# Optimization experiments

Measured on AMD Instinct MI355X. Metric: run time of the kernel, lower is better.

Reference implementation:

```python
import jax, jax.numpy as jnp
import numpy as np

N = 50000      # nodes
E = 800000     # edges (avg degree 16)
IN = 64        # in_channels
H = 128        # hidden_channels
OUT = 64       # out_channels
NS = 10        # n_samples
EPS = 1e-5     # BatchNorm eps


def _sage_conv(x, src, dst, Wl, bl, Wr):
    # PyG SAGEConv (mean aggr): lin_l(mean_neighbors) + lin_r(x)
    n = x.shape[0]
    deg = jax.ops.segment_sum(jnp.ones(src.shape[0], x.dtype), dst, num_segments=n)
    agg = jax.ops.segment_sum(x[src], dst, num_segments=n) / jnp.clip(deg, 1.0)[:, None]
    return agg @ Wl + bl + x @ Wr


def _batchnorm(x, gamma, beta):
    # training-mode BN forward (batch statistics), deterministic
    m = x.mean(axis=0)
    v = x.var(axis=0)
    return (x - m) * jax.lax.rsqrt(v + EPS) * gamma + beta


def setup_inputs() -> dict:
    key = jax.random.key(0)
    ks = jax.random.split(key, 40)
    w = lambda k, shape: (jax.random.normal(k, shape, jnp.float32) * 0.05)
    inp = {
        "x": jax.random.normal(ks[0], (N, IN), jnp.float32),
        "edge_index": jax.random.randint(ks[1], (2, E), 0, N, dtype=jnp.int32),
        "batch": jnp.zeros((N,), jnp.int32),
        "noise": jax.random.normal(ks[2], (NS, N, OUT), jnp.float32),
        # encoder1: SAGEConv(IN,H) + BN(H)
        "We1l": w(ks[3], (IN, H)), "be1": jnp.zeros((H,), jnp.float32), "We1r": w(ks[4], (IN, H)),
        "g1": jnp.ones((H,), jnp.float32), "b1": jnp.zeros((H,), jnp.float32),
        # encoder2: SAGEConv(H,2H) + BN(2H) + SAGEConv(2H,2*OUT)
        "We2l": w(ks[5], (H, 2 * H)), "be2": jnp.zeros((2 * H,), jnp.float32), "We2r": w(ks[6], (H, 2 * H)),
        "g2": jnp.ones((2 * H,), jnp.float32), "b2": jnp.zeros((2 * H,), jnp.float32),
        "We3l": w(ks[7], (2 * H, 2 * OUT)), "be3": jnp.zeros((2 * OUT,), jnp.float32), "We3r": w(ks[8], (2 * H, 2 * OUT)),
        # x1_transform: Linear(H, IN)
        "Wt": w(ks[9], (H, IN)), "bt": jnp.zeros((IN,), jnp.float32),
        # decoder1: Linear(OUT+IN, H) + BN(H); decoder2: Linear(H, IN)
        "Wd1": w(ks[10], (OUT + IN, H)), "bd1": jnp.zeros((H,), jnp.float32),
        "gd": jnp.ones((H,), jnp.float32), "bd": jnp.zeros((H,), jnp.float32),
        "Wd2": w(ks[11], (H, IN)), "bd2": jnp.zeros((IN,), jnp.float32),
        # SAGPooling score GNN = GraphConv(H, 1): lin_rel (bias) + lin_root (no bias)
        "Wp_rel": w(ks[12], (H, 1)), "bp": jnp.zeros((1,), jnp.float32), "Wp_root": w(ks[13], (H, 1)),
    }
    return inp


def reference(x, edge_index, batch, noise,
              We1l, be1, We1r, g1, b1,
              We2l, be2, We2r, g2, b2,
              We3l, be3, We3r,
              Wt, bt, Wd1, bd1, gd, bd, Wd2, bd2,
              Wp_rel, bp, Wp_root):
    src, dst = edge_index[0], edge_index[1]

    # ---- encode ----
    x1 = _batchnorm(jax.nn.relu(_sage_conv(x, src, dst, We1l, be1, We1r)), g1, b1)
    x2 = _batchnorm(jax.nn.relu(_sage_conv(x1, src, dst, We2l, be2, We2r)), g2, b2)
    ms = _sage_conv(x2, src, dst, We3l, be3, We3r)        # [N, 2*OUT]
    mean, log_std = ms[:, :OUT], ms[:, OUT:]

    # ---- reparameterize: avg of n_samples draws == mean + std * mean(eps) ----
    z = mean + jnp.exp(log_std) * noise.mean(axis=0)

    # ---- decode ----
    x1t = x1 @ Wt + bt                                    # [N, IN]
    h = jax.nn.relu(jnp.concatenate([z, x1t], axis=-1) @ Wd1 + bd1)
    h = _batchnorm(h, gd, bd)
    reconstruction = h @ Wd2 + bd2                        # [N, IN]

    # ---- SAGPooling (ratio=0.5) on x1 ----
    agg = jax.ops.segment_sum(x1[src], dst, num_segments=N)   # GraphConv add-aggr
    score = jnp.tanh((agg @ Wp_rel + bp + x1 @ Wp_root)[:, 0])  # [N]
    k = N // 2
    _, perm = jax.lax.top_k(score, k)                     # kept node indices (desc score)

    keep = jnp.zeros((N,), bool).at[perm].set(True)
    newidx = jnp.zeros((N,), jnp.int32).at[perm].set(jnp.arange(k, dtype=jnp.int32))
    edge_mask = keep[src] & keep[dst]                     # edges surviving the pooling
    ei_cg = newidx[edge_index]                            # [2, E], valid where edge_mask
    # unpool: map coarse indices back to original node ids; -1 marks dropped edges
    edge_index_unpooled = jnp.where(edge_mask[None, :], perm[ei_cg].astype(jnp.int32), -1)
    x_unpooled = x1[perm]                                 # [k, H]

    return (reconstruction, x_unpooled, edge_index_unpooled, edge_mask, mean, log_std, x1)
```

## Files before the change

### kernel.cpp

```cpp
#include <hip/hip_runtime.h>
#include <hip/hip_bf16.h>
#include <math.h>

#define NN 50000
#define EE 800000
#define KHALF 25000
#define NSAMP 1024
#define NBK (NSAMP+1)

typedef short bf16x8 __attribute__((ext_vector_type(8)));
typedef short sh4 __attribute__((ext_vector_type(4)));
typedef float f32x4 __attribute__((ext_vector_type(4)));

static __device__ inline unsigned short f2bf(float f){
  __hip_bfloat16 h = __float2bfloat16(f);
  return __builtin_bit_cast(unsigned short, h);
}
static __device__ inline float bf2f(unsigned short u){
  unsigned int x = ((unsigned int)u)<<16;
  return __builtin_bit_cast(float, x);
}

__global__ void k_hist(const int* __restrict__ dst, int* __restrict__ cnt, int E){
  int i = blockIdx.x*blockDim.x + threadIdx.x;
  if(i<E) atomicAdd(&cnt[dst[i]], 1);
}

__global__ void k_scan(const int* __restrict__ deg, int* __restrict__ rowptr, int n){
  __shared__ int sm[1024];
  int t = threadIdx.x;
  int chunk = (n + 1023) >> 10;
  int b = t*chunk; int e = b+chunk; if(b>n) b=n; if(e>n) e=n;
  int s=0;
  for(int i=b;i<e;i++) s += deg[i];
  sm[t]=s; __syncthreads();
  for(int off=1; off<1024; off<<=1){
    int add = (t>=off)? sm[t-off] : 0;
    __syncthreads();
    sm[t] += add;
    __syncthreads();
  }
  int run = sm[t]-s;
  for(int i=b;i<e;i++){ rowptr[i]=run; run += deg[i]; }
  if(t==1023) rowptr[n]=sm[1023];
}

__global__ void k_fill(const int* __restrict__ src, const int* __restrict__ dst,
                       const int* __restrict__ rowptr, int* __restrict__ cnt,
                       int* __restrict__ csr, int E){
  int i = blockIdx.x*blockDim.x + threadIdx.x;
  if(i<E){
    int d = dst[i];
    int p = rowptr[d] + atomicAdd(&cnt[d],1);
    csr[p] = src[i];
  }
}

template<typename AccT, typename OT, int F, int VW>
__global__ void k_segmean(const float* __restrict__ x, const int* __restrict__ csr,
                          const int* __restrict__ rowptr, OT* __restrict__ out, int n){
  int gid = blockIdx.x*blockDim.x + threadIdx.x;
  int node = gid >> 6; int lane = gid & 63;
  if(node>=n) return;
  int b = rowptr[node], e = rowptr[node+1];
  AccT acc[VW];
  #pragma unroll
  for(int k=0;k<VW;k++) acc[k]=(AccT)0;
  const float* xp = x + lane*VW;
  for(int j=b;j<e;j++){
    const float* row = xp + (long)csr[j]*F;
    if(VW==1){
      acc[0] += (AccT)row[0];
    } else if(VW==2){
      float2 v = *(const float2*)row;
      acc[0]+=(AccT)v.x; acc[1]+=(AccT)v.y;
    } else {
      float4 v = *(const float4*)row;
      acc[0]+=(AccT)v.x; acc[1]+=(AccT)v.y; acc[2]+=(AccT)v.z; acc[3]+=(AccT)v.w;
    }
  }
  int d = e-b; if(d<1) d=1;
  AccT inv = (AccT)1 / (AccT)d;
  #pragma unroll
  for(int k=0;k<VW;k++) out[(long)node*F + lane*VW + k] = (OT)(acc[k]*inv);
}

__global__ void k_segmean_bf(const unsigned short* __restrict__ xb,
                             const int* __restrict__ csr, const int* __restrict__ rowptr,
                             float* __restrict__ out, int n){
  int gid = blockIdx.x*blockDim.x + threadIdx.x;
  int node = gid >> 6; int lane = gid & 63;
  if(node>=n) return;
  int b = rowptr[node], e = rowptr[node+1];
  float a0=0.f, a1=0.f;
  const unsigned short* xp = xb + lane*2;
  for(int j=b;j<e;j++){
    unsigned int u = *(const unsigned int*)(xp + (long)csr[j]*128);
    a0 += bf2f((unsigned short)(u & 0xffff));
    a1 += bf2f((unsigned short)(u >> 16));
  }
  int d=e-b; if(d<1)d=1;
  float inv = 1.f/(float)d;
  float2 r; r.x=a0*inv; r.y=a1*inv;
  *(float2*)(out + (long)node*128 + lane*2) = r;
}

__global__ void k_segmean_ms(const unsigned short* __restrict__ T3,
                             const float* __restrict__ msr,
                             const int* __restrict__ csr, const int* __restrict__ rowptr,
                             float* __restrict__ omean, float* __restrict__ olstd, int n){
  int gid = blockIdx.x*blockDim.x + threadIdx.x;
  int node = gid >> 6; int lane = gid & 63;
  if(node>=n) return;
  int b = rowptr[node], e = rowptr[node+1];
  float a0=0.f, a1=0.f;
  const unsigned short* xp = T3 + lane*2;
  for(int j=b;j<e;j++){
    unsigned int u = *(const unsigned int*)(xp + (long)csr[j]*128);
    a0 += bf2f((unsigned short)(u & 0xffff));
    a1 += bf2f((unsigned short)(u >> 16));
  }
  int d=e-b; if(d<1)d=1;
  float inv = 1.f/(float)d;
  float2 mv = *(const float2*)(msr + (long)node*128 + lane*2);
  float2 r; r.x = a0*inv + mv.x; r.y = a1*inv + mv.y;
  int c0 = lane*2;
  if(c0 < 64) *(float2*)(omean + (long)node*64 + c0)      = r;
  else        *(float2*)(olstd + (long)node*64 + (c0-64)) = r;
}

static __device__ inline void stage_A_bf16(const float* __restrict__ P, int K, int k0,
                                           int m0, int M, int t,
                                           const float* __restrict__ bnsc,
                                           const float* __restrict__ bnsh,
                                           short* Ah, short* Al, bool bn){
  #pragma unroll
  for(int i=0;i<8;i++){
    int f4  = t + i*256;
    int row = f4 >> 4, c4 = f4 & 15;
    int gr  = m0 + row;
    float4 v = make_float4(0.f,0.f,0.f,0.f);
    if(gr < M) v = *(const float4*)(P + (long)gr*K + k0 + c4*4);
    if(bn){
      int kc = k0 + c4*4;
      v.x = v.x*bnsc[kc]   + bnsh[kc];
      v.y = v.y*bnsc[kc+1] + bnsh[kc+1];
      v.z = v.z*bnsc[kc+2] + bnsh[kc+2];
      v.w = v.w*bnsc[kc+3] + bnsh[kc+3];
    }
    unsigned short h0=f2bf(v.x), h1=f2bf(v.y), h2=f2bf(v.z), h3=f2bf(v.w);
    sh4 hi = (sh4){(short)h0,(short)h1,(short)h2,(short)h3};
    sh4 lo = (sh4){(short)f2bf(v.x-bf2f(h0)), (short)f2bf(v.y-bf2f(h1)),
                   (short)f2bf(v.z-bf2f(h2)), (short)f2bf(v.w-bf2f(h3))};
    int byte = (row*128 + c4*8) ^ ((row&7)<<4);
    *(sh4*)((char*)Ah + byte) = hi;
    *(sh4*)((char*)Al + byte) = lo;
  }
}

static __device__ inline void stage_B_bf16(const float* __restrict__ W, int J, int k0,
                                           int n0, int t, short* Bh, short* Bl){
  int n = t & 63, k4 = (t>>6)<<2;
  #pragma unroll
  for(int i=0;i<4;i++){
    int kb = i*16 + k4;
    const float* wp = W + (long)(k0+kb)*J + n0 + n;
    float w0 = wp[0], w1 = wp[J], w2 = wp[2*J], w3 = wp[3*J];
    unsigned short h0=f2bf(w0), h1=f2bf(w1), h2=f2bf(w2), h3=f2bf(w3);
    sh4 hi = (sh4){(short)h0,(short)h1,(short)h2,(short)h3};
    sh4 lo = (sh4){(short)f2bf(w0-bf2f(h0)), (short)f2bf(w1-bf2f(h1)),
                   (short)f2bf(w2-bf2f(h2)), (short)f2bf(w3-bf2f(h3))};
    int byte = (n*128 + kb*2) ^ ((n&7)<<4);
    *(sh4*)((char*)Bh + byte) = hi;
    *(sh4*)((char*)Bl + byte) = lo;
  }
}

__global__ __launch_bounds__(256) void k_gemm_bf16s(
    const float* __restrict__ A, const float* __restrict__ W1, int K1,
    const float* __restrict__ X, const float* __restrict__ W2, int K2,
    const float* __restrict__ bias, float* __restrict__ out,
    int M, int J, int relu,
    const float* __restrict__ bnsc, const float* __restrict__ bnsh)
{
  __shared__ __align__(16) short Ah[128*64];
  __shared__ __align__(16) short Al[128*64];
  __shared__ __align__(16) short Bh[64*64];
  __shared__ __align__(16) short Bl[64*64];
  const int m0 = blockIdx.x*128, n0 = blockIdx.y*64;
  const int t = threadIdx.x;
  const int lane = t & 63, wid = t >> 6;
  const int wm = wid >> 1, wn = wid & 1;

  f32x4 acc[4][2];
  #pragma unroll
  for(int i=0;i<4;i++)
    #pragma unroll
    for(int j=0;j<2;j++) acc[i][j] = (f32x4){0.f,0.f,0.f,0.f};

  const int ns1 = K1 >> 6;
  const int ns2 = X ? (K2 >> 6) : 0;
  for(int s=0; s<ns1+ns2; ++s){
    const float* P; const float* W; int K, k0;
    if(s < ns1){ P = A; W = W1; K = K1; k0 = s*64; }
    else       { P = X; W = W2; K = K2; k0 = (s-ns1)*64; }
    const bool bn = (bnsc != nullptr) && (s < ns1);

    stage_A_bf16(P, K, k0, m0, M, t, bnsc, bnsh, Ah, Al, bn);
    stage_B_bf16(W, J, k0, n0, t, Bh, Bl);
    __syncthreads();

    #pragma unroll
    for(int kk=0;kk<2;kk++){
      int kb = kk*32 + (lane>>4)*8;
      bf16x8 ahf[4], alf[4], bhf[2], blf[2];
      #pragma unroll
      for(int mf=0; mf<4; mf++){
        int r = wm*64 + mf*16 + (lane&15);
        int byte = (r*128 + kb*2) ^ ((r&7)<<4);
        ahf[mf] = *(const bf16x8*)((const char*)Ah + byte);
        alf[mf] = *(const bf16x8*)((const char*)Al + byte);
      }
      #pragma unroll
      for(int nf=0; nf<2; nf++){
        int n = wn*32 + nf*16 + (lane&15);
        int byte = (n*128 + kb*2) ^ ((n&7)<<4);
        bhf[nf] = *(const bf16x8*)((const char*)Bh + byte);
        blf[nf] = *(const bf16x8*)((const char*)Bl + byte);
      }
      #pragma unroll
      for(int mf=0; mf<4; mf++)
        #pragma unroll
        for(int nf=0; nf<2; nf++){
          acc[mf][nf] = __builtin_amdgcn_mfma_f32_16x16x32_bf16(ahf[mf], bhf[nf], acc[mf][nf], 0,0,0);
          acc[mf][nf] = __builtin_amdgcn_mfma_f32_16x16x32_bf16(ahf[mf], blf[nf], acc[mf][nf], 0,0,0);
          acc[mf][nf] = __builtin_amdgcn_mfma_f32_16x16x32_bf16(alf[mf], bhf[nf], acc[mf][nf], 0,0,0);
        }
    }
    __syncthreads();
  }

  #pragma unroll
  for(int mf=0; mf<4; mf++){
    #pragma unroll
    for(int nf=0; nf<2; nf++){
      int col = n0 + wn*32 + nf*16 + (lane&15);
      #pragma unroll
      for(int q=0;q<4;q++){
        int row = m0 + wm*64 + mf*16 + (lane>>4)*4 + q;
        if(row >= M) continue;
        float v = acc[mf][nf][q] + (bias ? bias[col] : 0.f);
        if(relu) v = fmaxf(v, 0.f);
        out[(long)row*J + col] = v;
      }
    }
  }
}

__global__ __launch_bounds__(256) void k_gemm_bf16s_2w(
    const float* __restrict__ A,
    const float* __restrict__ Wa, const float* __restrict__ Wb,
    const float* __restrict__ biasb,
    unsigned short* __restrict__ outa, float* __restrict__ outb,
    int M, int K,
    const float* __restrict__ bnsc, const float* __restrict__ bnsh)
{
  __shared__ __align__(16) short Ah[128*64];
  __shared__ __align__(16) short Al[128*64];
  __shared__ __align__(16) short Bh[64*64];
  __shared__ __align__(16) short Bl[64*64];
  const bool sel = blockIdx.y >= 2;
  const float* W = sel ? Wb : Wa;
  const int m0 = blockIdx.x*128, n0 = (blockIdx.y & 1)*64;
  const int t = threadIdx.x;
  const int lane = t & 63, wid = t >> 6;
  const int wm = wid >> 1, wn = wid & 1;

  f32x4 acc[4][2];
  #pragma unroll
  for(int i=0;i<4;i++)
    #pragma unroll
    for(int j=0;j<2;j++) acc[i][j] = (f32x4){0.f,0.f,0.f,0.f};

  const int ns1 = K >> 6;
  for(int s=0; s<ns1; ++s){
    int k0 = s*64;
    stage_A_bf16(A, K, k0, m0, M, t, bnsc, bnsh, Ah, Al, bnsc!=nullptr);
    stage_B_bf16(W, 128, k0, n0, t, Bh, Bl);
    __syncthreads();

    #pragma unroll
    for(int kk=0;kk<2;kk++){
      int kb = kk*32 + (lane>>4)*8;
      bf16x8 ahf[4], alf[4], bhf[2], blf[2];
      #pragma unroll
      for(int mf=0; mf<4; mf++){
        int r = wm*64 + mf*16 + (lane&15);
        int byte = (r*128 + kb*2) ^ ((r&7)<<4);
        ahf[mf] = *(const bf16x8*)((const char*)Ah + byte);
        alf[mf] = *(const bf16x8*)((const char*)Al + byte);
      }
      #pragma unroll
      for(int nf=0; nf<2; nf++){
        int n = wn*32 + nf*16 + (lane&15);
        int byte = (n*128 + kb*2) ^ ((n&7)<<4);
        bhf[nf] = *(const bf16x8*)((const char*)Bh + byte);
        blf[nf] = *(const bf16x8*)((const char*)Bl + byte);
      }
      #pragma unroll
      for(int mf=0; mf<4; mf++)
        #pragma unroll
        for(int nf=0; nf<2; nf++){
          acc[mf][nf] = __builtin_amdgcn_mfma_f32_16x16x32_bf16(ahf[mf], bhf[nf], acc[mf][nf], 0,0,0);
          acc[mf][nf] = __builtin_amdgcn_mfma_f32_16x16x32_bf16(ahf[mf], blf[nf], acc[mf][nf], 0,0,0);
          acc[mf][nf] = __builtin_amdgcn_mfma_f32_16x16x32_bf16(alf[mf], bhf[nf], acc[mf][nf], 0,0,0);
        }
    }
    __syncthreads();
  }

  #pragma unroll
  for(int mf=0; mf<4; mf++){
    #pragma unroll
    for(int nf=0; nf<2; nf++){
      int col = n0 + wn*32 + nf*16 + (lane&15);
      #pragma unroll
      for(int q=0;q<4;q++){
        int row = m0 + wm*64 + mf*16 + (lane>>4)*4 + q;
        if(row >= M) continue;
        if(sel){
          outb[(long)row*128 + col] = acc[mf][nf][q] + biasb[col];
        } else {
          outa[(long)row*128 + col] = f2bf(acc[mf][nf][q]);
        }
      }
    }
  }
}

__global__ __launch_bounds__(256) void k_gemm_c1(
    const double* __restrict__ A1, const float* __restrict__ X,
    const float* __restrict__ W1, const float* __restrict__ W2,
    const float* __restrict__ bias, double* __restrict__ out, int M)
{
  __shared__ double Asd[32*67];
  __shared__ float  Wsf[32*66];
  const int m0 = blockIdx.x*64, n0 = blockIdx.y*64;
  const int t = threadIdx.x;
  const int tm = t & 15, tn = t >> 4;
  double acc[4][4];
  #pragma unroll
  for(int i=0;i<4;i++)
    #pragma unroll
    for(int j=0;j<4;j++) acc[i][j]=0.0;

  for(int pair=0; pair<2; pair++){
    const float* Wp = pair ? W2 : W1;
    for(int k0=0; k0<64; k0+=32){
      #pragma unroll
      for(int i=0;i<8;i++){
        int idx = t + i*256;
        int r = idx >> 5, c = idx & 31;
        int gr = m0 + r;
        double v = 0.0;
        if(gr<M) v = pair ? (double)X[(long)gr*64 + k0 + c] : A1[(long)gr*64 + k0 + c];
        Asd[c*67 + r] = v;
      }
      #pragma unroll
      for(int i=0;i<8;i++){
        int idx = t + i*256;
        int kk = idx >> 6, n = idx & 63;
        Wsf[kk*66 + n] = Wp[(k0+kk)*128 + n0 + n];
      }
      __syncthreads();
      #pragma unroll
      for(int kk=0;kk<32;kk++){
        double a0=Asd[kk*67 + tm],    a1=Asd[kk*67 + tm+16];
        double a2=Asd[kk*67 + tm+32], a3=Asd[kk*67 + tm+48];
        double w0=(double)Wsf[kk*66 + tn*4+0], w1=(double)Wsf[kk*66 + tn*4+1];
        double w2=(double)Wsf[kk*66 + tn*4+2], w3=(double)Wsf[kk*66 + tn*4+3];
        acc[0][0] += a0*w0; acc[0][1] += a0*w1; acc[0][2] += a0*w2; acc[0][3] += a0*w3;
        acc[1][0] += a1*w0; acc[1][1] += a1*w1; acc[1][2] += a1*w2; acc[1][3] += a1*w3;
        acc[2][0] += a2*w0; acc[2][1] += a2*w1; acc[2][2] += a2*w2; acc[2][3] += a2*w3;
        acc[3][0] += a3*w0; acc[3][1] += a3*w1; acc[3][2] += a3*w2; acc[3][3] += a3*w3;
      }
      __syncthreads();
    }
  }
  #pragma unroll
  for(int i=0;i<4;i++){
    int gr = m0 + tm + 16*i;
    if(gr>=M) continue;
    #pragma unroll
    for(int j=0;j<4;j++){
      int gc = n0 + tn*4 + j;
      double v = acc[i][j] + (double)bias[gc];
      if(v<0.0) v=0.0;
      out[(long)gr*128 + gc] = v;
    }
  }
}

__global__ void k_wfold(const float* __restrict__ Wt, const float* __restrict__ bt,
                        const float* __restrict__ Wd1, const float* __restrict__ bd1,
                        float* __restrict__ Wc, float* __restrict__ bc){
  int j = threadIdx.x;
  int i = blockIdx.x;
  float s;
  if(i < 128){
    s = 0.f;
    for(int k=0;k<64;k++) s += Wt[i*64+k] * Wd1[(64+k)*128 + j];
    Wc[i*128+j] = s;
  } else {
    s = bd1[j];
    for(int k=0;k<64;k++) s += bt[k] * Wd1[(64+k)*128 + j];
    bc[j] = s;
  }
}

template<typename T>
__global__ void k_colstats(const T* __restrict__ x, int M, int J,
                           double* __restrict__ ps, double* __restrict__ pq){
  int c = threadIdx.x; int b = blockIdx.x, B = gridDim.x;
  int rows = (M + B - 1)/B;
  int r0 = b*rows, r1 = r0+rows; if(r1>M) r1=M;
  double s=0.0,q=0.0;
  for(int r=r0;r<r1;r++){ double v = (double)x[(long)r*J + c]; s+=v; q+=v*v; }
  ps[(long)b*J+c]=s; pq[(long)b*J+c]=q;
}

__global__ void k_bnfinal(const double* __restrict__ ps, const double* __restrict__ pq,
                          int B, int J, int M, const float* __restrict__ g,
                          const float* __restrict__ bta,
                          double* __restrict__ sc, double* __restrict__ sh,
                          float* __restrict__ sc32, float* __restrict__ sh32){
  int c = threadIdx.x; if(c>=J) return;
  double s=0.0,q=0.0;
  for(int b=0;b<B;b++){ s+=ps[(long)b*J+c]; q+=pq[(long)b*J+c]; }
  double m = s/M; double v = q/M - m*m;
  double inv = 1.0/sqrt(v + 1e-5);
  double a = (double)g[c]*inv;
  sc[c]=a; sh[c]=(double)bta[c] - m*a;
  sc32[c]=(float)a; sh32[c]=(float)((double)bta[c] - m*a);
}

__global__ void k_bntr(const double* __restrict__ xp,
                       const double* __restrict__ sc, const double* __restrict__ sh,
                       const float* __restrict__ wrel, const float* __restrict__ wroot,
                       float* __restrict__ o32, unsigned short* __restrict__ obf,
                       double* __restrict__ t, double* __restrict__ r, int n){
  int gid = blockIdx.x*blockDim.x + threadIdx.x;
  int node = gid>>6, lane = gid&63;
  if(node>=n) return;
  long base = (long)node*128;
  double v0 = xp[base+lane]   *sc[lane]    + sh[lane];
  double v1 = xp[base+lane+64]*sc[lane+64] + sh[lane+64];
  float f0 = (float)v0, f1 = (float)v1;
  o32[base+lane]    = f0;
  o32[base+lane+64] = f1;
  obf[base+lane]    = f2bf(f0);
  obf[base+lane+64] = f2bf(f1);
  double tv = v0*(double)wrel[lane]  + v1*(double)wrel[lane+64];
  double rv = v0*(double)wroot[lane] + v1*(double)wroot[lane+64];
  for(int off=32; off>0; off>>=1){
    tv += __shfl_xor(tv, off);
    rv += __shfl_xor(rv, off);
  }
  if(lane==0){ t[node]=tv; r[node]=rv; }
}

__global__ void k_z(const float* __restrict__ mean, const float* __restrict__ lstd,
                    const float* __restrict__ noise, float* __restrict__ z, int total4){
  int i = blockIdx.x*blockDim.x + threadIdx.x;
  if(i>=total4) return;
  const float4* m4 = (const float4*)mean;
  const float4* l4 = (const float4*)lstd;
  const float4* n4 = (const float4*)noise;
  float4 m = m4[i], l = l4[i];
  float nx=0.f, ny=0.f, nz=0.f, nw=0.f;
  #pragma unroll
  for(int s=0;s<10;s++){
    float4 v = n4[(long)s*total4 + i];
    nx+=v.x; ny+=v.y; nz+=v.z; nw+=v.w;
  }
  float4 o;
  o.x = (float)((double)m.x + exp((double)l.x)*((double)nx*0.1));
  o.y = (float)((double)m.y + exp((double)l.y)*((double)ny*0.1));
  o.z = (float)((double)m.z + exp((double)l.z)*((double)nz*0.1));
  o.w = (float)((double)m.w + exp((double)l.w)*((double)nw*0.1));
  ((float4*)z)[i] = o;
}

__global__ void k_score(const double* __restrict__ t, const double* __restrict__ r,
                        const int* __restrict__ csr, const int* __restrict__ rowptr,
                        const float* __restrict__ bp,
                        unsigned long long* __restrict__ key, int n){
  int i = blockIdx.x*blockDim.x + threadIdx.x;
  if(i>=n) return;
  double s = (double)bp[0] + r[i];
  int b=rowptr[i], e=rowptr[i+1];
  for(int j=b;j<e;j++) s += t[csr[j]];
  double sc = tanh(s) + 0.0;
  long long u = __double_as_longlong(sc);
  unsigned long long uu = (unsigned long long)u;
  key[i] = (u < 0) ? ~uu : (uu ^ 0x8000000000000000ULL);
}

__global__ void k_sample_sort(const unsigned long long* __restrict__ key,
                              unsigned long long* __restrict__ samp){
  __shared__ unsigned long long sm[NSAMP];
  int t = threadIdx.x;
  sm[t] = key[t*48];
  __syncthreads();
  for(int k=2; k<=NSAMP; k<<=1){
    for(int j=k>>1; j>0; j>>=1){
      int l = t ^ j;
      if(l > t){
        unsigned long long a = sm[t], b = sm[l];
        bool up = ((t & k) == 0);
        if(up ? (a > b) : (a < b)){ sm[t]=b; sm[l]=a; }
      }
      __syncthreads();
    }
  }
  samp[t] = sm[t];
}

__global__ __launch_bounds__(256) void k_bucket_assign(
    const unsigned long long* __restrict__ key,
    const unsigned long long* __restrict__ samp,
    int* __restrict__ bucket, int* __restrict__ bcnt, int n){
  __shared__ unsigned long long sm[NSAMP];
  for(int u=threadIdx.x; u<NSAMP; u+=256) sm[u] = samp[u];
  __syncthreads();
  int i = blockIdx.x*256 + threadIdx.x;
  if(i>=n) return;
  unsigned long long ki = key[i];
  int lo=0, hi=NSAMP;
  while(lo<hi){ int mid=(lo+hi)>>1; if(sm[mid] < ki) lo=mid+1; else hi=mid; }
  bucket[i]=lo;
  atomicAdd(&bcnt[lo],1);
}

__global__ void k_bucket_fill(const int* __restrict__ bucket,
                              const int* __restrict__ bstart, int* __restrict__ bfill,
                              int* __restrict__ blist, int n){
  int i = blockIdx.x*blockDim.x + threadIdx.x;
  if(i>=n) return;
  int b = bucket[i];
  int p = bstart[b] + atomicAdd(&bfill[b],1);
  blist[p] = i;
}

__global__ __launch_bounds__(256) void k_bucket_rank(
    const unsigned long long* __restrict__ key,
    const int* __restrict__ blist, const int* __restrict__ bstart,
    int n, int k, int* __restrict__ keep, int* __restrict__ perm){
  __shared__ unsigned long long skey[2048];
  __shared__ int sidx[2048];
  int b = blockIdx.x;
  int s0 = bstart[b], s1 = bstart[b+1];
  int m = s1 - s0;
  if(m<=0) return;
  int above = n - s1;
  if(m <= 2048){
    for(int u=threadIdx.x; u<m; u+=256){ int ii=blist[s0+u]; sidx[u]=ii; skey[u]=key[ii]; }
    __syncthreads();
    for(int u=threadIdx.x; u<m; u+=256){
      unsigned long long ki = skey[u]; int ii = sidx[u];
      int c = 0;
      for(int v=0; v<m; v++){
        unsigned long long kv = skey[v];
        c += ((kv > ki) || (kv == ki && sidx[v] < ii)) ? 1 : 0;
      }
      int rank = above + c;
      int kp = (rank < k) ? 1 : 0;
      keep[ii] = kp;
      if(kp) perm[rank] = ii;
    }
  } else {
    for(int u=threadIdx.x; u<m; u+=256){
      int ii = blist[s0+u];
      unsigned long long ki = key[ii];
      int c=0;
      for(int v=0; v<m; v++){
        int jj = blist[s0+v];
        unsigned long long kv = key[jj];
        c += ((kv > ki) || (kv == ki && jj < ii)) ? 1 : 0;
      }
      int rank = above + c;
      int kp = (rank < k) ? 1 : 0;
      keep[ii] = kp;
      if(kp) perm[rank] = ii;
    }
  }
}

__global__ void k_unpool(const float* __restrict__ x1, const int* __restrict__ perm,
                         float* __restrict__ out, int k){
  int i = blockIdx.x*blockDim.x + threadIdx.x;
  if(i >= k*128) return;
  int r = i>>7, c = i&127;
  out[i] = x1[(long)perm[r]*128 + c];
}

__global__ void k_edgeout(const int* __restrict__ src, const int* __restrict__ dst,
                          const int* __restrict__ keep, float* __restrict__ o2,
                          float* __restrict__ o3, int E){
  int e = blockIdx.x*blockDim.x + threadIdx.x;
  if(e>=E) return;
  int s=src[e], d=dst[e];
  bool m = keep[s] && keep[d];
  o2[e]   = m ? (float)s : -1.f;
  o2[E+e] = m ? (float)d : -1.f;
  o3[e]   = m ? 1.f : 0.f;
}

extern "C" void kernel_launch(void* const* d_in, const int* in_sizes, int n_in,
                              void* d_out, int out_size, void* d_ws, size_t ws_size,
                              hipStream_t stream){
  const float* x     = (const float*)d_in[0];
  const int*   ei    = (const int*)d_in[1];
  const float* noise = (const float*)d_in[3];
  const float* We1l  = (const float*)d_in[4];
  const float* be1   = (const float*)d_in[5];
  const float* We1r  = (const float*)d_in[6];
  const float* g1    = (const float*)d_in[7];
  const float* b1    = (const float*)d_in[8];
  const float* We2l  = (const float*)d_in[9];
  const float* be2   = (const float*)d_in[10];
  const float* We2r  = (const float*)d_in[11];
  const float* g2    = (const float*)d_in[12];
  const float* b2    = (const float*)d_in[13];
  const float* We3l  = (const float*)d_in[14];
  const float* be3   = (const float*)d_in[15];
  const float* We3r  = (const float*)d_in[16];
  const float* Wt    = (const float*)d_in[17];
  const float* bt    = (const float*)d_in[18];
  const float* Wd1   = (const float*)d_in[19];
  const float* bd1   = (const float*)d_in[20];
  const float* gd    = (const float*)d_in[21];
  const float* bd    = (const float*)d_in[22];
  const float* Wd2   = (const float*)d_in[23];
  const float* bd2   = (const float*)d_in[24];
  const float* Wprel = (const float*)d_in[25];
  const float* bp    = (const float*)d_in[26];
  const float* Wproot= (const float*)d_in[27];

  const int* src = ei;
  const int* dst = ei + EE;

  float* out   = (float*)d_out;
  float* o_rec  = out;
  float* o_xun  = out + 3200000;
  float* o_eiu  = out + 6400000;
  float* o_mask = out + 8000000;
  float* o_mean = out + 8800000;
  float* o_lstd = out + 12000000;
  float* o_x1   = out + 15200000;

  char* w = (char*)d_ws;
  size_t off = 0;
  auto alloc = [&](size_t bytes)->char*{
    char* p = w + off; off += (bytes + 255) & ~(size_t)255; return p;
  };
  int*    csr  = (int*)   alloc((size_t)EE*4);
  int*    rowp = (int*)   alloc((size_t)(NN+1)*4);
  int*    cnt  = (int*)   alloc((size_t)NN*4);
  char*   B3   =          alloc((size_t)NN*128*8);
  char*   B4   =          alloc((size_t)NN*64*8);
  char*   B5   =          alloc((size_t)NN*256*4);
  double* t_   = (double*)alloc((size_t)NN*8);
  double* r_   = (double*)alloc((size_t)NN*8);
  unsigned long long* key_ = (unsigned long long*)alloc((size_t)NN*8);
  int*    keep = (int*)   alloc((size_t)NN*4);
  int*    perm = (int*)   alloc((size_t)KHALF*4);
  double* ps   = (double*)alloc((size_t)240*256*8);
  double* pq   = (double*)alloc((size_t)240*256*8);
  double* bnsc = (double*)alloc(256*8);
  double* bnsh = (double*)alloc(256*8);
  float*  sc1f = (float*) alloc(256*4);
  float*  sh1f = (float*) alloc(256*4);
  float*  sc2f = (float*) alloc(256*4);
  float*  sh2f = (float*) alloc(256*4);
  float*  scdf = (float*) alloc(256*4);
  float*  shdf = (float*) alloc(256*4);
  float*  Wc   = (float*) alloc((size_t)128*128*4);
  float*  bc   = (float*) alloc(128*4);
  unsigned long long* samp = (unsigned long long*)alloc((size_t)NSAMP*8);
  int*    bucket = (int*) alloc((size_t)NN*4);
  int*    bcnt   = (int*) alloc((size_t)NBK*4);
  int*    bstart = (int*) alloc((size_t)(NBK+1)*4);
  int*    bfill  = (int*) alloc((size_t)NBK*4);
  int*    blist  = (int*) alloc((size_t)NN*4);
  (void)in_sizes; (void)n_in; (void)out_size; (void)ws_size;

  double* A1  = (double*)B4;
  double* x1p = (double*)B3;
  float*  A2  = (float*)B4;
  float*  x2  = (float*)B3;
  unsigned short* x1bf = (unsigned short*)B5;
  unsigned short* T3   = (unsigned short*)B5;
  float*  msr = (float*)(B5 + (size_t)NN*128*4);
  float*  zb  = (float*)B5;
  float*  h   = (float*)B4;

  const int GX = (NN+127)/128;

  hipMemsetAsync(cnt, 0, (size_t)NN*4, stream);
  k_hist<<<(EE+255)/256,256,0,stream>>>(dst, cnt, EE);
  k_wfold<<<129,128,0,stream>>>(Wt, bt, Wd1, bd1, Wc, bc);
  k_scan<<<1,1024,0,stream>>>(cnt, rowp, NN);
  hipMemsetAsync(cnt, 0, (size_t)NN*4, stream);
  k_fill<<<(EE+255)/256,256,0,stream>>>(src, dst, rowp, cnt, csr, EE);

  k_segmean<double,double,64,1><<<(NN+3)/4,256,0,stream>>>(x, csr, rowp, A1, NN);
  { dim3 g((NN+63)/64, 2);
    k_gemm_c1<<<g,256,0,stream>>>(A1, x, We1l, We1r, be1, x1p, NN); }
  k_colstats<double><<<240,128,0,stream>>>(x1p, NN, 128, ps, pq);
  k_bnfinal<<<1,128,0,stream>>>(ps,pq,240,128,NN,g1,b1,bnsc,bnsh,sc1f,sh1f);
  k_bntr<<<(NN+3)/4,256,0,stream>>>(x1p, bnsc, bnsh, Wprel, Wproot, o_x1, x1bf, t_, r_, NN);

  k_segmean_bf<<<(NN+3)/4,256,0,stream>>>(x1bf, csr, rowp, A2, NN);
  { dim3 g(GX, 4);
    k_gemm_bf16s<<<g,256,0,stream>>>(A2, We2l, 128, o_x1, We2r, 128, be2, x2, NN, 256, 1, nullptr, nullptr); }
  k_colstats<float><<<240,256,0,stream>>>(x2, NN, 256, ps, pq);
  k_bnfinal<<<1,256,0,stream>>>(ps,pq,240,256,NN,g2,b2,bnsc,bnsh,sc2f,sh2f);

  { dim3 g(GX, 4);
    k_gemm_bf16s_2w<<<g,256,0,stream>>>(x2, We3l, We3r, be3, T3, msr, NN, 256, sc2f, sh2f); }
  k_segmean_ms<<<(NN+3)/4,256,0,stream>>>(T3, msr, csr, rowp, o_mean, o_lstd, NN);

  k_z<<<(800000+255)/256,256,0,stream>>>(o_mean, o_lstd, noise, zb, 800000);
  { dim3 g(GX, 2);
    k_gemm_bf16s<<<g,256,0,stream>>>(zb, Wd1, 64, o_x1, Wc, 128, bc, h, NN, 128, 1, nullptr, nullptr); }
  k_colstats<float><<<240,128,0,stream>>>(h, NN, 128, ps, pq);
  k_bnfinal<<<1,128,0,stream>>>(ps,pq,240,128,NN,gd,bd,bnsc,bnsh,scdf,shdf);
  { dim3 g(GX, 1);
    k_gemm_bf16s<<<g,256,0,stream>>>(h, Wd2, 128, nullptr, nullptr, 0, bd2, o_rec, NN, 64, 0, scdf, shdf); }

  k_score<<<(NN+255)/256,256,0,stream>>>(t_, r_, csr, rowp, bp, key_, NN);
  k_sample_sort<<<1,1024,0,stream>>>(key_, samp);
  hipMemsetAsync(bcnt, 0, (size_t)NBK*4, stream);
  k_bucket_assign<<<(NN+255)/256,256,0,stream>>>(key_, samp, bucket, bcnt, NN);
  k_scan<<<1,1024,0,stream>>>(bcnt, bstart, NBK);
  hipMemsetAsync(bfill, 0, (size_t)NBK*4, stream);
  k_bucket_fill<<<(NN+255)/256,256,0,stream>>>(bucket, bstart, bfill, blist, NN);
  k_bucket_rank<<<NBK,256,0,stream>>>(key_, blist, bstart, NN, KHALF, keep, perm);
  k_unpool<<<(KHALF*128+255)/256,256,0,stream>>>(o_x1, perm, o_xun, KHALF);
  k_edgeout<<<(EE+255)/256,256,0,stream>>>(src, dst, keep, o_eiu, o_mask, EE);
}
```

Measured before the change: 1.220 ms.

## Pre-split activations and weights into bf16 hi/lo planes before GEMMs

```diff
diff --git a/kernel.cpp b/kernel.cpp
--- a/kernel.cpp
+++ b/kernel.cpp
@@ -9,7 +9,8 @@
 #define NBK (NSAMP+1)
 
 typedef short bf16x8 __attribute__((ext_vector_type(8)));
-typedef short sh4 __attribute__((ext_vector_type(4)));
+typedef unsigned short us8 __attribute__((ext_vector_type(8)));
+typedef unsigned short us4 __attribute__((ext_vector_type(4)));
 typedef float f32x4 __attribute__((ext_vector_type(4)));
 
 static __device__ inline unsigned short f2bf(float f){
@@ -69,25 +70,17 @@
   const float* xp = x + lane*VW;
   for(int j=b;j<e;j++){
     const float* row = xp + (long)csr[j]*F;
-    if(VW==1){
-      acc[0] += (AccT)row[0];
-    } else if(VW==2){
-      float2 v = *(const float2*)row;
-      acc[0]+=(AccT)v.x; acc[1]+=(AccT)v.y;
-    } else {
-      float4 v = *(const float4*)row;
-      acc[0]+=(AccT)v.x; acc[1]+=(AccT)v.y; acc[2]+=(AccT)v.z; acc[3]+=(AccT)v.w;
-    }
+    acc[0] += (AccT)row[0];
   }
   int d = e-b; if(d<1) d=1;
   AccT inv = (AccT)1 / (AccT)d;
-  #pragma unroll
-  for(int k=0;k<VW;k++) out[(long)node*F + lane*VW + k] = (OT)(acc[k]*inv);
-}
-
-__global__ void k_segmean_bf(const unsigned short* __restrict__ xb,
-                             const int* __restrict__ csr, const int* __restrict__ rowptr,
-                             float* __restrict__ out, int n){
+  out[(long)node*F + lane] = (OT)(acc[0]*inv);
+}
+
+__global__ void k_segmean_bfp(const unsigned short* __restrict__ xb,
+                              const int* __restrict__ csr, const int* __restrict__ rowptr,
+                              unsigned short* __restrict__ a2h, unsigned short* __restrict__ a2l,
+                              int n){
   int gid = blockIdx.x*blockDim.x + threadIdx.x;
   int node = gid >> 6; int lane = gid & 63;
   if(node>=n) return;
@@ -101,8 +94,12 @@
   }
   int d=e-b; if(d<1)d=1;
   float inv = 1.f/(float)d;
-  float2 r; r.x=a0*inv; r.y=a1*inv;
-  *(float2*)(out + (long)node*128 + lane*2) = r;
+  float rx = a0*inv, ry = a1*inv;
+  unsigned short hx=f2bf(rx), hy=f2bf(ry);
+  unsigned short lx=f2bf(rx-bf2f(hx)), ly=f2bf(ry-bf2f(hy));
+  long o = (long)node*128 + lane*2;
+  *(unsigned int*)(a2h + o) = (unsigned int)hx | ((unsigned int)hy<<16);
+  *(unsigned int*)(a2l + o) = (unsigned int)lx | ((unsigned int)ly<<16);
 }
 
 __global__ void k_segmean_ms(const unsigned short* __restrict__ T3,
@@ -129,59 +126,52 @@
   else        *(float2*)(olstd + (long)node*64 + (c0-64)) = r;
 }
 
-static __device__ inline void stage_A_bf16(const float* __restrict__ P, int K, int k0,
-                                           int m0, int M, int t,
-                                           const float* __restrict__ bnsc,
-                                           const float* __restrict__ bnsh,
-                                           short* Ah, short* Al, bool bn){
-  #pragma unroll
-  for(int i=0;i<8;i++){
-    int f4  = t + i*256;
-    int row = f4 >> 4, c4 = f4 & 15;
+static __device__ inline void stage_A_ps(const unsigned short* __restrict__ AH,
+                                         const unsigned short* __restrict__ AL,
+                                         int K, int k0, int m0, int M, int t,
+                                         short* Ah, short* Al){
+  #pragma unroll
+  for(int i=0;i<4;i++){
+    int f8 = t + i*256;
+    int row = f8 >> 3, c8 = f8 & 7;
     int gr  = m0 + row;
-    float4 v = make_float4(0.f,0.f,0.f,0.f);
-    if(gr < M) v = *(const float4*)(P + (long)gr*K + k0 + c4*4);
-    if(bn){
-      int kc = k0 + c4*4;
-      v.x = v.x*bnsc[kc]   + bnsh[kc];
-      v.y = v.y*bnsc[kc+1] + bnsh[kc+1];
-      v.z = v.z*bnsc[kc+2] + bnsh[kc+2];
-      v.w = v.w*bnsc[kc+3] + bnsh[kc+3];
-    }
-    unsigned short h0=f2bf(v.x), h1=f2bf(v.y), h2=f2bf(v.z), h3=f2bf(v.w);
-    sh4 hi = (sh4){(short)h0,(short)h1,(short)h2,(short)h3};
-    sh4 lo = (sh4){(short)f2bf(v.x-bf2f(h0)), (short)f2bf(v.y-bf2f(h1)),
-                   (short)f2bf(v.z-bf2f(h2)), (short)f2bf(v.w-bf2f(h3))};
-    int byte = (row*128 + c4*8) ^ ((row&7)<<4);
-    *(sh4*)((char*)Ah + byte) = hi;
-    *(sh4*)((char*)Al + byte) = lo;
-  }
-}
-
-static __device__ inline void stage_B_bf16(const float* __restrict__ W, int J, int k0,
-                                           int n0, int t, short* Bh, short* Bl){
-  int n = t & 63, k4 = (t>>6)<<2;
-  #pragma unroll
-  for(int i=0;i<4;i++){
-    int kb = i*16 + k4;
-    const float* wp = W + (long)(k0+kb)*J + n0 + n;
-    float w0 = wp[0], w1 = wp[J], w2 = wp[2*J], w3 = wp[3*J];
-    unsigned short h0=f2bf(w0), h1=f2bf(w1), h2=f2bf(w2), h3=f2bf(w3);
-    sh4 hi = (sh4){(short)h0,(short)h1,(short)h2,(short)h3};
-    sh4 lo = (sh4){(short)f2bf(w0-bf2f(h0)), (short)f2bf(w1-bf2f(h1)),
-                   (short)f2bf(w2-bf2f(h2)), (short)f2bf(w3-bf2f(h3))};
+    us8 vh = (us8){0,0,0,0,0,0,0,0};
+    us8 vl = (us8){0,0,0,0,0,0,0,0};
+    if(gr < M){
+      long base = (long)gr*K + k0 + c8*8;
+      vh = *(const us8*)(AH + base);
+      vl = *(const us8*)(AL + base);
+    }
+    int byte = (row*128 + c8*16) ^ ((row&7)<<4);
+    *(us8*)((char*)Ah + byte) = vh;
+    *(us8*)((char*)Al + byte) = vl;
+  }
+}
+
+static __device__ inline void stage_B_ps(const unsigned short* __restrict__ WH,
+                                         const unsigned short* __restrict__ WL,
+                                         int K, int k0, int n0, int t,
+                                         short* Bh, short* Bl){
+  int n = t & 63, k8 = (t>>6)<<3;
+  #pragma unroll
+  for(int i=0;i<2;i++){
+    int kb = i*32 + k8;
+    long base = (long)(n0+n)*K + k0 + kb;
+    us8 vh = *(const us8*)(WH + base);
+    us8 vl = *(const us8*)(WL + base);
     int byte = (n*128 + kb*2) ^ ((n&7)<<4);
-    *(sh4*)((char*)Bh + byte) = hi;
-    *(sh4*)((char*)Bl + byte) = lo;
-  }
-}
-
-__global__ __launch_bounds__(256) void k_gemm_bf16s(
-    const float* __restrict__ A, const float* __restrict__ W1, int K1,
-    const float* __restrict__ X, const float* __restrict__ W2, int K2,
+    *(us8*)((char*)Bh + byte) = vh;
+    *(us8*)((char*)Bl + byte) = vl;
+  }
+}
+
+__global__ __launch_bounds__(256) void k_gemm_ps(
+    const unsigned short* __restrict__ AH, const unsigned short* __restrict__ AL, int K1,
+    const unsigned short* __restrict__ XH, const unsigned short* __restrict__ XL, int K2,
+    const unsigned short* __restrict__ W1H, const unsigned short* __restrict__ W1L,
+    const unsigned short* __restrict__ W2H, const unsigned short* __restrict__ W2L,
     const float* __restrict__ bias, float* __restrict__ out,
-    int M, int J, int relu,
-    const float* __restrict__ bnsc, const float* __restrict__ bnsh)
+    int M, int J, int relu)
 {
   __shared__ __align__(16) short Ah[128*64];
   __shared__ __align__(16) short Al[128*64];
@@ -199,15 +189,14 @@
     for(int j=0;j<2;j++) acc[i][j] = (f32x4){0.f,0.f,0.f,0.f};
 
   const int ns1 = K1 >> 6;
-  const int ns2 = X ? (K2 >> 6) : 0;
+  const int ns2 = XH ? (K2 >> 6) : 0;
   for(int s=0; s<ns1+ns2; ++s){
-    const float* P; const float* W; int K, k0;
-    if(s < ns1){ P = A; W = W1; K = K1; k0 = s*64; }
-    else       { P = X; W = W2; K = K2; k0 = (s-ns1)*64; }
-    const bool bn = (bnsc != nullptr) && (s < ns1);
-
-    stage_A_bf16(P, K, k0, m0, M, t, bnsc, bnsh, Ah, Al, bn);
-    stage_B_bf16(W, J, k0, n0, t, Bh, Bl);
+    const unsigned short *PH, *PL, *WH, *WL; int K, k0;
+    if(s < ns1){ PH=AH; PL=AL; K=K1; k0=s*64; WH=W1H; WL=W1L; }
+    else       { PH=XH; PL=XL; K=K2; k0=(s-ns1)*64; WH=W2H; WL=W2L; }
+
+    stage_A_ps(PH, PL, K, k0, m0, M, t, Ah, Al);
+    stage_B_ps(WH, WL, K, k0, n0, t, Bh, Bl);
     __syncthreads();
 
     #pragma unroll
@@ -257,20 +246,20 @@
   }
 }
 
-__global__ __launch_bounds__(256) void k_gemm_bf16s_2w(
-    const float* __restrict__ A,
-    const float* __restrict__ Wa, const float* __restrict__ Wb,
+__global__ __launch_bounds__(256) void k_gemm_ps2w(
+    const unsigned short* __restrict__ AH, const unsigned short* __restrict__ AL, int K,
+    const unsigned short* __restrict__ WaH, const unsigned short* __restrict__ WaL,
+    const unsigned short* __restrict__ WbH, const unsigned short* __restrict__ WbL,
     const float* __restrict__ biasb,
-    unsigned short* __restrict__ outa, float* __restrict__ outb,
-    int M, int K,
-    const float* __restrict__ bnsc, const float* __restrict__ bnsh)
+    unsigned short* __restrict__ outa, float* __restrict__ outb, int M)
 {
   __shared__ __align__(16) short Ah[128*64];
   __shared__ __align__(16) short Al[128*64];
   __shared__ __align__(16) short Bh[64*64];
   __shared__ __align__(16) short Bl[64*64];
   const bool sel = blockIdx.y >= 2;
-  const float* W = sel ? Wb : Wa;
+  const unsigned short* WH = sel ? WbH : WaH;
+  const unsigned short* WL = sel ? WbL : WaL;
   const int m0 = blockIdx.x*128, n0 = (blockIdx.y & 1)*64;
   const int t = threadIdx.x;
   const int lane = t & 63, wid = t >> 6;
@@ -282,11 +271,11 @@
     #pragma unroll
     for(int j=0;j<2;j++) acc[i][j] = (f32x4){0.f,0.f,0.f,0.f};
 
-  const int ns1 = K >> 6;
-  for(int s=0; s<ns1; ++s){
+  const int ns = K >> 6;
+  for(int s=0; s<ns; ++s){
     int k0 = s*64;
-    stage_A_bf16(A, K, k0, m0, M, t, bnsc, bnsh, Ah, Al, bnsc!=nullptr);
-    stage_B_bf16(W, 128, k0, n0, t, Bh, Bl);
+    stage_A_ps(AH, AL, K, k0, m0, M, t, Ah, Al);
+    stage_B_ps(WH, WL, K, k0, n0, t, Bh, Bl);
     __syncthreads();
 
     #pragma unroll
@@ -328,17 +317,14 @@
       for(int q=0;q<4;q++){
         int row = m0 + wm*64 + mf*16 + (lane>>4)*4 + q;
         if(row >= M) continue;
-        if(sel){
-          outb[(long)row*128 + col] = acc[mf][nf][q] + biasb[col];
-        } else {
-          outa[(long)row*128 + col] = f2bf(acc[mf][nf][q]);
-        }
-      }
-    }
-  }
-}
-
-__global__ __launch_bounds__(256) void k_gemm_c1(
+        if(sel) outb[(long)row*128 + col] = acc[mf][nf][q] + biasb[col];
+        else    outa[(long)row*128 + col] = f2bf(acc[mf][nf][q]);
+      }
+    }
+  }
+}
+
+__global__ __launch_bounds__(256,5) void k_gemm_c1(
     const double* __restrict__ A1, const float* __restrict__ X,
     const float* __restrict__ W1, const float* __restrict__ W2,
     const float* __restrict__ bias, double* __restrict__ out, int M)
@@ -403,18 +389,53 @@
 
 __global__ void k_wfold(const float* __restrict__ Wt, const float* __restrict__ bt,
                         const float* __restrict__ Wd1, const float* __restrict__ bd1,
-                        float* __restrict__ Wc, float* __restrict__ bc){
+                        unsigned short* __restrict__ WcTh, unsigned short* __restrict__ WcTl,
+                        float* __restrict__ bc){
   int j = threadIdx.x;
   int i = blockIdx.x;
-  float s;
   if(i < 128){
-    s = 0.f;
+    float s = 0.f;
     for(int k=0;k<64;k++) s += Wt[i*64+k] * Wd1[(64+k)*128 + j];
-    Wc[i*128+j] = s;
+    unsigned short h = f2bf(s);
+    WcTh[j*128 + i] = h;
+    WcTl[j*128 + i] = f2bf(s - bf2f(h));
   } else {
-    s = bd1[j];
+    float s = bd1[j];
     for(int k=0;k<64;k++) s += bt[k] * Wd1[(64+k)*128 + j];
     bc[j] = s;
+  }
+}
+
+static __device__ inline void wsplit1(const float* __restrict__ W, int kshift, int J,
+                                      unsigned short* __restrict__ oh,
+                                      unsigned short* __restrict__ ol, int idx){
+  int total = J << kshift;
+  if(idx >= total) return;
+  int K = 1 << kshift;
+  int n = idx >> kshift, k = idx & (K-1);
+  float v = W[k*J + n];
+  unsigned short h = f2bf(v);
+  oh[idx] = h;
+  ol[idx] = f2bf(v - bf2f(h));
+}
+
+__global__ void k_wsplit(const float* We2l, const float* We2r,
+                         const float* We3l, const float* We3r,
+                         const float* Wd1, const float* Wd2,
+                         unsigned short* e2lh, unsigned short* e2ll,
+                         unsigned short* e2rh, unsigned short* e2rl,
+                         unsigned short* e3lh, unsigned short* e3ll,
+                         unsigned short* e3rh, unsigned short* e3rl,
+                         unsigned short* d1h, unsigned short* d1l,
+                         unsigned short* d2h, unsigned short* d2l){
+  int idx = blockIdx.x*256 + threadIdx.x;
+  switch(blockIdx.y){
+    case 0: wsplit1(We2l, 7, 256, e2lh, e2ll, idx); break;
+    case 1: wsplit1(We2r, 7, 256, e2rh, e2rl, idx); break;
+    case 2: wsplit1(We3l, 8, 128, e3lh, e3ll, idx); break;
+    case 3: wsplit1(We3r, 8, 128, e3rh, e3rl, idx); break;
+    case 4: wsplit1(Wd1,  6, 128, d1h,  d1l,  idx); break;
+    case 5: wsplit1(Wd2,  7, 64,  d2h,  d2l,  idx); break;
   }
 }
 
@@ -444,10 +465,31 @@
   sc32[c]=(float)a; sh32[c]=(float)((double)bta[c] - m*a);
 }
 
+__global__ void k_bnsplit(const float* __restrict__ x, const float* __restrict__ sc,
+                          const float* __restrict__ sh,
+                          unsigned short* __restrict__ oh, unsigned short* __restrict__ ol,
+                          int total4, int Jm){
+  int i = blockIdx.x*256 + threadIdx.x;
+  if(i>=total4) return;
+  float4 v = ((const float4*)x)[i];
+  int c = (i*4) & Jm;
+  v.x = v.x*sc[c]   + sh[c];
+  v.y = v.y*sc[c+1] + sh[c+1];
+  v.z = v.z*sc[c+2] + sh[c+2];
+  v.w = v.w*sc[c+3] + sh[c+3];
+  unsigned short h0=f2bf(v.x), h1=f2bf(v.y), h2=f2bf(v.z), h3=f2bf(v.w);
+  us4 hi = (us4){h0,h1,h2,h3};
+  us4 lo = (us4){f2bf(v.x-bf2f(h0)), f2bf(v.y-bf2f(h1)),
+                 f2bf(v.z-bf2f(h2)), f2bf(v.w-bf2f(h3))};
+  ((us4*)oh)[i] = hi;
+  ((us4*)ol)[i] = lo;
+}
+
 __global__ void k_bntr(const double* __restrict__ xp,
                        const double* __restrict__ sc, const double* __restrict__ sh,
                        const float* __restrict__ wrel, const float* __restrict__ wroot,
-                       float* __restrict__ o32, unsigned short* __restrict__ obf,
+                       float* __restrict__ o32,
+                       unsigned short* __restrict__ x1h, unsigned short* __restrict__ x1l,
                        double* __restrict__ t, double* __restrict__ r, int n){
   int gid = blockIdx.x*blockDim.x + threadIdx.x;
   int node = gid>>6, lane = gid&63;
@@ -458,8 +500,11 @@
   float f0 = (float)v0, f1 = (float)v1;
   o32[base+lane]    = f0;
   o32[base+lane+64] = f1;
-  obf[base+lane]    = f2bf(f0);
-  obf[base+lane+64] = f2bf(f1);
+  unsigned short h0 = f2bf(f0), h1 = f2bf(f1);
+  x1h[base+lane]    = h0;
+  x1h[base+lane+64] = h1;
+  x1l[base+lane]    = f2bf(f0 - bf2f(h0));
+  x1l[base+lane+64] = f2bf(f1 - bf2f(h1));
   double tv = v0*(double)wrel[lane]  + v1*(double)wrel[lane+64];
   double rv = v0*(double)wroot[lane] + v1*(double)wroot[lane+64];
   for(int off=32; off>0; off>>=1){
@@ -470,7 +515,9 @@
 }
 
 __global__ void k_z(const float* __restrict__ mean, const float* __restrict__ lstd,
-                    const float* __restrict__ noise, float* __restrict__ z, int total4){
+                    const float* __restrict__ noise,
+                    unsigned short* __restrict__ zh, unsigned short* __restrict__ zl,
+                    int total4){
   int i = blockIdx.x*blockDim.x + threadIdx.x;
   if(i>=total4) return;
   const float4* m4 = (const float4*)mean;
@@ -483,12 +530,16 @@
     float4 v = n4[(long)s*total4 + i];
     nx+=v.x; ny+=v.y; nz+=v.z; nw+=v.w;
   }
-  float4 o;
-  o.x = (float)((double)m.x + exp((double)l.x)*((double)nx*0.1));
-  o.y = (float)((double)m.y + exp((double)l.y)*((double)ny*0.1));
-  o.z = (float)((double)m.z + exp((double)l.z)*((double)nz*0.1));
-  o.w = (float)((double)m.w + exp((double)l.w)*((double)nw*0.1));
-  ((float4*)z)[i] = o;
+  float o0 = (float)((double)m.x + exp((double)l.x)*((double)nx*0.1));
+  float o1 = (float)((double)m.y + exp((double)l.y)*((double)ny*0.1));
+  float o2 = (float)((double)m.z + exp((double)l.z)*((double)nz*0.1));
+  float o3 = (float)((double)m.w + exp((double)l.w)*((double)nw*0.1));
+  unsigned short h0=f2bf(o0), h1=f2bf(o1), h2=f2bf(o2), h3=f2bf(o3);
+  us4 hi = (us4){h0,h1,h2,h3};
+  us4 lo = (us4){f2bf(o0-bf2f(h0)), f2bf(o1-bf2f(h1)),
+                 f2bf(o2-bf2f(h2)), f2bf(o3-bf2f(h3))};
+  ((us4*)zh)[i] = hi;
+  ((us4*)zl)[i] = lo;
 }
 
 __global__ void k_score(const double* __restrict__ t, const double* __restrict__ r,
@@ -670,6 +721,8 @@
   char*   B3   =          alloc((size_t)NN*128*8);
   char*   B4   =          alloc((size_t)NN*64*8);
   char*   B5   =          alloc((size_t)NN*256*4);
+  unsigned short* x1h = (unsigned short*)alloc((size_t)NN*128*2);
+  unsigned short* x1l = (unsigned short*)alloc((size_t)NN*128*2);
   double* t_   = (double*)alloc((size_t)NN*8);
   double* r_   = (double*)alloc((size_t)NN*8);
   unsigned long long* key_ = (unsigned long long*)alloc((size_t)NN*8);
@@ -685,8 +738,21 @@
   float*  sh2f = (float*) alloc(256*4);
   float*  scdf = (float*) alloc(256*4);
   float*  shdf = (float*) alloc(256*4);
-  float*  Wc   = (float*) alloc((size_t)128*128*4);
+  unsigned short* WcTh = (unsigned short*)alloc(128*128*2);
+  unsigned short* WcTl = (unsigned short*)alloc(128*128*2);
   float*  bc   = (float*) alloc(128*4);
+  unsigned short* e2lh = (unsigned short*)alloc(128*256*2);
+  unsigned short* e2ll = (unsigned short*)alloc(128*256*2);
+  unsigned short* e2rh = (unsigned short*)alloc(128*256*2);
+  unsigned short* e2rl = (unsigned short*)alloc(128*256*2);
+  unsigned short* e3lh = (unsigned short*)alloc(256*128*2);
+  unsigned short* e3ll = (unsigned short*)alloc(256*128*2);
+  unsigned short* e3rh = (unsigned short*)alloc(256*128*2);
+  unsigned short* e3rl = (unsigned short*)alloc(256*128*2);
+  unsigned short* d1h  = (unsigned short*)alloc(64*128*2);
+  unsigned short* d1l  = (unsigned short*)alloc(64*128*2);
+  unsigned short* d2h  = (unsigned short*)alloc(128*64*2);
+  unsigned short* d2l  = (unsigned short*)alloc(128*64*2);
   unsigned long long* samp = (unsigned long long*)alloc((size_t)NSAMP*8);
   int*    bucket = (int*) alloc((size_t)NN*4);
   int*    bcnt   = (int*) alloc((size_t)NBK*4);
@@ -696,20 +762,29 @@
   (void)in_sizes; (void)n_in; (void)out_size; (void)ws_size;
 
   double* A1  = (double*)B4;
+  unsigned short* a2h = (unsigned short*)B4;
+  unsigned short* a2l = a2h + (size_t)NN*128;
+  unsigned short* hh  = (unsigned short*)B4;
+  unsigned short* hl  = hh + (size_t)NN*128;
   double* x1p = (double*)B3;
-  float*  A2  = (float*)B4;
   float*  x2  = (float*)B3;
-  unsigned short* x1bf = (unsigned short*)B5;
-  unsigned short* T3   = (unsigned short*)B5;
-  float*  msr = (float*)(B5 + (size_t)NN*128*4);
-  float*  zb  = (float*)B5;
-  float*  h   = (float*)B4;
+  unsigned short* T3 = (unsigned short*)B3;
+  float*  msr = (float*)(B3 + (size_t)NN*128*2);
+  float*  h   = (float*)B3;
+  unsigned short* x2h = (unsigned short*)B5;
+  unsigned short* x2l = x2h + (size_t)NN*256;
+  unsigned short* zh  = (unsigned short*)B5;
+  unsigned short* zl  = zh + (size_t)NN*64;
 
   const int GX = (NN+127)/128;
 
   hipMemsetAsync(cnt, 0, (size_t)NN*4, stream);
   k_hist<<<(EE+255)/256,256,0,stream>>>(dst, cnt, EE);
-  k_wfold<<<129,128,0,stream>>>(Wt, bt, Wd1, bd1, Wc, bc);
+  k_wfold<<<129,128,0,stream>>>(Wt, bt, Wd1, bd1, WcTh, WcTl, bc);
+  { dim3 g(128, 6);
+    k_wsplit<<<g,256,0,stream>>>(We2l, We2r, We3l, We3r, Wd1, Wd2,
+                                 e2lh,e2ll, e2rh,e2rl, e3lh,e3ll, e3rh,e3rl,
+                                 d1h,d1l, d2h,d2l); }
   k_scan<<<1,1024,0,stream>>>(cnt, rowp, NN);
   hipMemsetAsync(cnt, 0, (size_t)NN*4, stream);
   k_fill<<<(EE+255)/256,256,0,stream>>>(src, dst, rowp, cnt, csr, EE);
@@ -719,25 +794,30 @@
     k_gemm_c1<<<g,256,0,stream>>>(A1, x, We1l, We1r, be1, x1p, NN); }
   k_colstats<double><<<240,128,0,stream>>>(x1p, NN, 128, ps, pq);
   k_bnfinal<<<1,128,0,stream>>>(ps,pq,240,128,NN,g1,b1,bnsc,bnsh,sc1f,sh1f);
-  k_bntr<<<(NN+3)/4,256,0,stream>>>(x1p, bnsc, bnsh, Wprel, Wproot, o_x1, x1bf, t_, r_, NN);
-
-  k_segmean_bf<<<(NN+3)/4,256,0,stream>>>(x1bf, csr, rowp, A2, NN);
+  k_bntr<<<(NN+3)/4,256,0,stream>>>(x1p, bnsc, bnsh, Wprel, Wproot, o_x1, x1h, x1l, t_, r_, NN);
+
+  k_segmean_bfp<<<(NN+3)/4,256,0,stream>>>(x1h, csr, rowp, a2h, a2l, NN);
   { dim3 g(GX, 4);
-    k_gemm_bf16s<<<g,256,0,stream>>>(A2, We2l, 128, o_x1, We2r, 128, be2, x2, NN, 256, 1, nullptr, nullptr); }
+    k_gemm_ps<<<g,256,0,stream>>>(a2h,a2l,128, x1h,x1l,128,
+                                  e2lh,e2ll, e2rh,e2rl, be2, x2, NN, 256, 1); }
   k_colstats<float><<<240,256,0,stream>>>(x2, NN, 256, ps, pq);
   k_bnfinal<<<1,256,0,stream>>>(ps,pq,240,256,NN,g2,b2,bnsc,bnsh,sc2f,sh2f);
 
+  k_bnsplit<<<(3200000+255)/256,256,0,stream>>>(x2, sc2f, sh2f, x2h, x2l, 3200000, 255);
   { dim3 g(GX, 4);
-    k_gemm_bf16s_2w<<<g,256,0,stream>>>(x2, We3l, We3r, be3, T3, msr, NN, 256, sc2f, sh2f); }
+    k_gemm_ps2w<<<g,256,0,stream>>>(x2h,x2l,256, e3lh,e3ll, e3rh,e3rl, be3, T3, msr, NN); }
   k_segmean_ms<<<(NN+3)/4,256,0,stream>>>(T3, msr, csr, rowp, o_mean, o_lstd, NN);
 
-  k_z<<<(800000+255)/256,256,0,stream>>>(o_mean, o_lstd, noise, zb, 800000);
+  k_z<<<(800000+255)/256,256,0,stream>>>(o_mean, o_lstd, noise, zh, zl, 800000);
   { dim3 g(GX, 2);
-    k_gemm_bf16s<<<g,256,0,stream>>>(zb, Wd1, 64, o_x1, Wc, 128, bc, h, NN, 128, 1, nullptr, nullptr); }
+    k_gemm_ps<<<g,256,0,stream>>>(zh,zl,64, x1h,x1l,128,
+                                  d1h,d1l, WcTh,WcTl, bc, h, NN, 128, 1); }
   k_colstats<float><<<240,128,0,stream>>>(h, NN, 128, ps, pq);
   k_bnfinal<<<1,128,0,stream>>>(ps,pq,240,128,NN,gd,bd,bnsc,bnsh,scdf,shdf);
+  k_bnsplit<<<(1600000+255)/256,256,0,stream>>>(h, scdf, shdf, hh, hl, 1600000, 127);
   { dim3 g(GX, 1);
-    k_gemm_bf16s<<<g,256,0,stream>>>(h, Wd2, 128, nullptr, nullptr, 0, bd2, o_rec, NN, 64, 0, scdf, shdf); }
+    k_gemm_ps<<<g,256,0,stream>>>(hh,hl,128, nullptr,nullptr,0,
+                                  d2h,d2l, nullptr,nullptr, bd2, o_rec, NN, 64, 0); }
 
   k_score<<<(NN+255)/256,256,0,stream>>>(t_, r_, csr, rowp, bp, key_, NN);
   k_sample_sort<<<1,1024,0,stream>>>(key_, samp);
```

After: 1.254 ms. 2.8% more time.
